# Optimization experiments

Hardware: AMD Instinct MI355X
Metric: run time of the kernel (lower is better)

## Reference

```python
import jax, jax.numpy as jnp
import numpy as np

EMBED = 1024
HEADS = 16
HEAD_DIM = EMBED // HEADS
HIDDEN = int(EMBED * 4.0)
EPS = 1e-6


def setup_inputs() -> dict:
    key = jax.random.key(0)
    ks = jax.random.split(key, 8)
    s = lambda fan_in: 1.0 / np.sqrt(fan_in)
    x = jax.random.normal(ks[0], (2, 2048, EMBED), dtype=jnp.float32)
    return {
        "x": x,
        "ln1_g": jnp.ones((EMBED,), jnp.float32),
        "ln1_b": jnp.zeros((EMBED,), jnp.float32),
        "w_qkv": jax.random.normal(ks[1], (EMBED, 3 * EMBED), jnp.float32) * s(EMBED),
        "b_qkv": jnp.zeros((3 * EMBED,), jnp.float32),
        "w_proj": jax.random.normal(ks[2], (EMBED, EMBED), jnp.float32) * s(EMBED),
        "b_proj": jnp.zeros((EMBED,), jnp.float32),
        "ln2_g": jnp.ones((EMBED,), jnp.float32),
        "ln2_b": jnp.zeros((EMBED,), jnp.float32),
        "w_fc1": jax.random.normal(ks[3], (EMBED, HIDDEN), jnp.float32) * s(EMBED),
        "b_fc1": jnp.zeros((HIDDEN,), jnp.float32),
        "w_fc2": jax.random.normal(ks[4], (HIDDEN, EMBED), jnp.float32) * s(HIDDEN),
        "b_fc2": jnp.zeros((EMBED,), jnp.float32),
    }


def _layernorm(x, g, b):
    mu = jnp.mean(x, axis=-1, keepdims=True)
    var = jnp.mean(jnp.square(x - mu), axis=-1, keepdims=True)
    return (x - mu) * jax.lax.rsqrt(var + EPS) * g + b


def _attention(x, w_qkv, b_qkv, w_proj, b_proj):
    B, N, C = x.shape
    qkv = x @ w_qkv + b_qkv                      # [B,N,3C]
    qkv = qkv.reshape(B, N, 3, HEADS, HEAD_DIM)
    q, k, v = (qkv[:, :, 0], qkv[:, :, 1], qkv[:, :, 2])  # [B,N,H,Dh]
    scale = HEAD_DIM ** -0.5
    attn = jnp.einsum('bnhd,bmhd->bhnm', q, k) * scale     # [B,H,N,N]
    attn = jax.nn.softmax(attn, axis=-1)
    out = jnp.einsum('bhnm,bmhd->bnhd', attn, v).reshape(B, N, C)
    return out @ w_proj + b_proj


def reference(x, ln1_g, ln1_b, w_qkv, b_qkv, w_proj, b_proj,
              ln2_g, ln2_b, w_fc1, b_fc1, w_fc2, b_fc2):
    x = x + _attention(_layernorm(x, ln1_g, ln1_b), w_qkv, b_qkv, w_proj, b_proj)
    h = _layernorm(x, ln2_g, ln2_b)
    h = jax.nn.gelu(h @ w_fc1 + b_fc1, approximate=False)
    x = x + (h @ w_fc2 + b_fc2)
    return x
```

## Files before the change

### kernel.cpp

```cpp
#include <hip/hip_runtime.h>
#include <hip/hip_bf16.h>
#include <math.h>

typedef __bf16 bf16x8 __attribute__((ext_vector_type(8)));
typedef __bf16 bf16x4 __attribute__((ext_vector_type(4)));
typedef unsigned short u16x8 __attribute__((ext_vector_type(8)));
typedef float f32x4 __attribute__((ext_vector_type(4)));

#define EP_QKV 0
#define EP_GELU 1
#define EP_RES 2

static __device__ __forceinline__ unsigned short f2bf(float x) {
  unsigned int u = __float_as_uint(x);
  unsigned int r = (u + 0x7fffu + ((u >> 16) & 1u)) >> 16;
  return (unsigned short)r;
}

static __device__ __forceinline__ unsigned int pkbf(float lo, float hi) {
  return __builtin_amdgcn_perm(__float_as_uint(hi), __float_as_uint(lo), 0x07060302);
}

static __device__ __forceinline__ void async16(const void* g, void* l) {
  __builtin_amdgcn_global_load_lds((__attribute__((address_space(1))) void*)g,
                                   (__attribute__((address_space(3))) void*)l, 16, 0, 0);
}

__global__ __launch_bounds__(256) void wt_transpose(const float* __restrict__ in,
                                                    unsigned short* __restrict__ out,
                                                    int K, int N) {
  __shared__ float tile[32][33];
  const int n0 = blockIdx.x * 32;
  const int k0 = blockIdx.y * 32;
  const int tx = threadIdx.x;
  const int ty = threadIdx.y;
  #pragma unroll
  for (int i = ty; i < 32; i += 8)
    tile[i][tx] = in[(size_t)(k0 + i) * N + n0 + tx];
  __syncthreads();
  #pragma unroll
  for (int i = ty; i < 32; i += 8)
    out[(size_t)(n0 + i) * K + k0 + tx] = f2bf(tile[tx][i]);
}

__global__ __launch_bounds__(256) void ln_kernel(const float* __restrict__ x,
                                                 const float* __restrict__ g,
                                                 const float* __restrict__ b,
                                                 unsigned short* __restrict__ outp) {
  const int row = blockIdx.x;
  const int tid = threadIdx.x;
  const int wave = tid >> 6, lane = tid & 63;
  const float4 v = ((const float4*)(x + (size_t)row * 1024))[tid];
  float s = v.x + v.y + v.z + v.w;
  #pragma unroll
  for (int i = 1; i < 64; i <<= 1) s += __shfl_xor(s, i);
  __shared__ float red[4];
  if (lane == 0) red[wave] = s;
  __syncthreads();
  const float mean = (red[0] + red[1] + red[2] + red[3]) * (1.f / 1024.f);
  const float dx = v.x - mean, dy = v.y - mean, dz = v.z - mean, dw = v.w - mean;
  float ss = dx * dx + dy * dy + dz * dz + dw * dw;
  #pragma unroll
  for (int i = 1; i < 64; i <<= 1) ss += __shfl_xor(ss, i);
  __syncthreads();
  if (lane == 0) red[wave] = ss;
  __syncthreads();
  const float var = (red[0] + red[1] + red[2] + red[3]) * (1.f / 1024.f);
  const float inv = rsqrtf(var + 1e-6f);
  const float4 gv = ((const float4*)g)[tid];
  const float4 bv = ((const float4*)b)[tid];
  ushort4 o;
  o.x = f2bf(dx * inv * gv.x + bv.x);
  o.y = f2bf(dy * inv * gv.y + bv.y);
  o.z = f2bf(dz * inv * gv.z + bv.z);
  o.w = f2bf(dw * inv * gv.w + bv.w);
  ((ushort4*)(outp + (size_t)row * 1024))[tid] = o;
}

template <int TN>
__global__ __launch_bounds__(256) void gemm_kernel(
    const unsigned short* __restrict__ A,
    const unsigned short* __restrict__ BT,
    const float* __restrict__ bias,
    int M, int N, int K, int mode,
    void* __restrict__ outp, const float* __restrict__ res) {
  constexpr int AM = (TN == 128) ? 4 : 2;
  constexpr int BCH = TN / 64;
  __shared__ __align__(16) char smem[16384 + 2 * TN * 64];

  const int tid = threadIdx.x;
  const int wave = tid >> 6, lane = tid & 63;
  const int quad = lane >> 4, l16 = lane & 15;
  const int wm = (TN == 128) ? (wave >> 1) : wave;
  const int wn = (TN == 128) ? (wave & 1) : 0;
  const int bn = blockIdx.x, bm = blockIdx.y;
  const int row_m = bm * 128, row_n = bn * TN;

  int ar[2], ac[2];
  #pragma unroll
  for (int i = 0; i < 2; ++i) {
    const int c = wave * 128 + i * 64 + lane;
    ar[i] = c >> 2;
    ac[i] = ((c & 3) ^ (ar[i] & 3)) * 8;
  }
  int br[BCH], bc[BCH];
  #pragma unroll
  for (int i = 0; i < BCH; ++i) {
    const int c = wave * (64 * BCH) + i * 64 + lane;
    br[i] = c >> 2;
    bc[i] = ((c & 3) ^ (br[i] & 3)) * 8;
  }

  const unsigned short* Ag = A + (size_t)row_m * K;
  const unsigned short* Bg = BT + (size_t)row_n * K;

  const f32x4 z = {0.f, 0.f, 0.f, 0.f};
  f32x4 acc[AM][4];
  #pragma unroll
  for (int i = 0; i < AM; ++i)
    #pragma unroll
    for (int j = 0; j < 4; ++j) acc[i][j] = z;

  auto issue = [&](int kt, int b) {
    unsigned short* As = (unsigned short*)(smem + b * 8192);
    unsigned short* Bs = (unsigned short*)(smem + 16384 + b * TN * 64);
    #pragma unroll
    for (int i = 0; i < 2; ++i)
      async16(Ag + (size_t)ar[i] * K + kt + ac[i], As + wave * 1024 + i * 512);
    #pragma unroll
    for (int i = 0; i < BCH; ++i)
      async16(Bg + (size_t)br[i] * K + kt + bc[i], Bs + wave * (BCH * 512) + i * 512);
  };

  issue(0, 0);
  for (int kt = 0; kt < K; kt += 32) {
    const int b = (kt >> 5) & 1;
    __syncthreads();
    if (kt + 32 < K) issue(kt + 32, b ^ 1);
    const unsigned short* As = (const unsigned short*)(smem + b * 8192);
    const unsigned short* Bs = (const unsigned short*)(smem + 16384 + b * TN * 64);
    bf16x8 af[AM], bfv[4];
    #pragma unroll
    for (int t = 0; t < AM; ++t) {
      const int row = wm * (AM * 16) + t * 16 + l16;
      const int ch = quad ^ (row & 3);
      af[t] = *(const bf16x8*)(As + row * 32 + ch * 8);
    }
    #pragma unroll
    for (int t = 0; t < 4; ++t) {
      const int row = wn * 64 + t * 16 + l16;
      const int ch = quad ^ (row & 3);
      bfv[t] = *(const bf16x8*)(Bs + row * 32 + ch * 8);
    }
    #pragma unroll
    for (int tm = 0; tm < AM; ++tm)
      #pragma unroll
      for (int tn = 0; tn < 4; ++tn)
        acc[tm][tn] = __builtin_amdgcn_mfma_f32_16x16x32_bf16(af[tm], bfv[tn], acc[tm][tn], 0, 0, 0);
  }

  #pragma unroll
  for (int tn = 0; tn < 4; ++tn) {
    const int col = row_n + wn * 64 + tn * 16 + l16;
    const float bv = bias[col];
    #pragma unroll
    for (int tm = 0; tm < AM; ++tm) {
      const int rbase = row_m + wm * (AM * 16) + tm * 16 + quad * 4;
      float v[4];
      #pragma unroll
      for (int r = 0; r < 4; ++r) v[r] = acc[tm][tn][r] + bv;
      if (mode == EP_QKV) {
        unsigned short* outw = (unsigned short*)outp;
        const int which = col >> 10;
        const int h = (col >> 6) & 15, d = col & 63;
        const int bb = rbase >> 11, n = rbase & 2047;
        const size_t bh = (size_t)(bb * 16 + h);
        if (which == 0) {
          #pragma unroll
          for (int r = 0; r < 4; ++r)
            outw[(bh * 2048 + n + r) * 64 + d] = f2bf(v[r] * 0.125f);
        } else if (which == 1) {
          #pragma unroll
          for (int r = 0; r < 4; ++r)
            outw[4194304ull + (bh * 2048 + n + r) * 64 + d] = f2bf(v[r]);
        } else {
          uint2 o;
          o.x = pkbf(v[0], v[1]);
          o.y = pkbf(v[2], v[3]);
          *(uint2*)(outw + 8388608ull + (bh * 64 + d) * 2048 + n) = o;
        }
      } else if (mode == EP_GELU) {
        #pragma unroll
        for (int r = 0; r < 4; ++r) {
          const float u = v[r];
          const float c = 1.5957691216f * fmaf(0.044715f * u * u, u, u);
          const float e = __expf(c);
          const float gl = u - __fdividef(u, e + 1.0f);
          ((unsigned short*)outp)[(size_t)(rbase + r) * N + col] = f2bf(gl);
        }
      } else {
        #pragma unroll
        for (int r = 0; r < 4; ++r)
          ((float*)outp)[(size_t)(rbase + r) * N + col] =
              res[(size_t)(rbase + r) * N + col] + v[r];
      }
    }
  }
}

__global__ __launch_bounds__(256) void attn_kernel(
    const unsigned short* __restrict__ Q,
    const unsigned short* __restrict__ Kb,
    const unsigned short* __restrict__ VT,
    unsigned short* __restrict__ outp) {
  __shared__ __align__(16) char smem[40960];
  unsigned short* Qs = (unsigned short*)smem;
  unsigned short* Ks = (unsigned short*)(smem + 8192);
  unsigned short* Vs = (unsigned short*)(smem + 24576);

  const int tid = threadIdx.x;
  const int wave = tid >> 6, lane = tid & 63;
  const int quad = lane >> 4, l16 = lane & 15;
  const int bhi = blockIdx.y;
  const int q0 = blockIdx.x * 64;

  const unsigned short* Qg = Q + ((size_t)bhi * 2048 + q0) * 64;
  const unsigned short* Kg = Kb + (size_t)bhi * 2048 * 64;
  const unsigned short* Vg = VT + (size_t)bhi * 64 * 2048;

  {
    const int c0 = wave * 128 + lane;
    const int r0 = c0 >> 3, k0 = ((c0 & 7) ^ (r0 & 7)) * 8;
    const int c1 = c0 + 64;
    const int r1 = c1 >> 3, k1 = ((c1 & 7) ^ (r1 & 7)) * 8;
    async16(Qg + r0 * 64 + k0, Qs + wave * 1024);
    async16(Qg + r1 * 64 + k1, Qs + wave * 1024 + 512);
  }
  __syncthreads();

  bf16x8 qb[4][2];
  #pragma unroll
  for (int nt = 0; nt < 4; ++nt)
    #pragma unroll
    for (int h = 0; h < 2; ++h) {
      const int row = nt * 16 + l16;
      const int ch = (h * 4 + quad) ^ (row & 7);
      qb[nt][h] = *(const bf16x8*)(Qs + row * 64 + ch * 8);
    }

  int kr[4], kc[4], vr[4], vc[4];
  #pragma unroll
  for (int i = 0; i < 4; ++i) {
    const int c = wave * 256 + i * 64 + lane;
    kr[i] = c >> 3;
    kc[i] = ((c & 7) ^ (kr[i] & 7)) * 8;
    vr[i] = c >> 4;
    vc[i] = ((c & 15) ^ (vr[i] & 15)) * 8;
  }

  const f32x4 z = {0.f, 0.f, 0.f, 0.f};
  f32x4 acc[4][4];
  #pragma unroll
  for (int i = 0; i < 4; ++i)
    #pragma unroll
    for (int j = 0; j < 4; ++j) acc[i][j] = z;
  float lsum[4] = {0.f, 0.f, 0.f, 0.f};

  const int rowA = wave * 16 + l16;
  const int rowB = 64 + rowA;
  const int swk = l16 & 7;

  for (int kt = 0; kt < 2048; kt += 128) {
    #pragma unroll
    for (int i = 0; i < 4; ++i)
      async16(Kg + (size_t)(kt + kr[i]) * 64 + kc[i], Ks + wave * 2048 + i * 512);
    #pragma unroll
    for (int i = 0; i < 4; ++i)
      async16(Vg + (size_t)vr[i] * 2048 + kt + vc[i], Vs + wave * 2048 + i * 512);
    __syncthreads();

    f32x4 sA[4], sB[4];
    #pragma unroll
    for (int nt = 0; nt < 4; ++nt) { sA[nt] = z; sB[nt] = z; }
    #pragma unroll
    for (int h = 0; h < 2; ++h) {
      const int ch = (h * 4 + quad) ^ swk;
      bf16x8 kfA = *(const bf16x8*)(Ks + rowA * 64 + ch * 8);
      bf16x8 kfB = *(const bf16x8*)(Ks + rowB * 64 + ch * 8);
      #pragma unroll
      for (int nt = 0; nt < 4; ++nt) {
        sA[nt] = __builtin_amdgcn_mfma_f32_16x16x32_bf16(kfA, qb[nt][h], sA[nt], 0, 0, 0);
        sB[nt] = __builtin_amdgcn_mfma_f32_16x16x32_bf16(kfB, qb[nt][h], sB[nt], 0, 0, 0);
      }
    }

    bf16x8 pb[4];
    #pragma unroll
    for (int nt = 0; nt < 4; ++nt) {
      union { unsigned int d[4]; bf16x8 b; } cv;
      float pa[4], pv[4];
      float ls = 0.f;
      #pragma unroll
      for (int r = 0; r < 4; ++r) {
        pa[r] = __expf(sA[nt][r] - 16.0f);
        pv[r] = __expf(sB[nt][r] - 16.0f);
        ls += pa[r] + pv[r];
      }
      cv.d[0] = pkbf(pa[0], pa[1]);
      cv.d[1] = pkbf(pa[2], pa[3]);
      cv.d[2] = pkbf(pv[0], pv[1]);
      cv.d[3] = pkbf(pv[2], pv[3]);
      lsum[nt] += ls;
      pb[nt] = cv.b;
    }

    #pragma unroll
    for (int mt = 0; mt < 4; ++mt) {
      const int d = mt * 16 + l16;
      const int cA = (wave * 2 + (quad >> 1)) ^ (d & 15);
      const int cB = (8 + wave * 2 + (quad >> 1)) ^ (d & 15);
      const int sub = (quad & 1) * 4;
      bf16x4 vA = *(const bf16x4*)(Vs + d * 128 + cA * 8 + sub);
      bf16x4 vB = *(const bf16x4*)(Vs + d * 128 + cB * 8 + sub);
      bf16x8 vf = __builtin_shufflevector(vA, vB, 0, 1, 2, 3, 4, 5, 6, 7);
      #pragma unroll
      for (int nt = 0; nt < 4; ++nt)
        acc[mt][nt] = __builtin_amdgcn_mfma_f32_16x16x32_bf16(vf, pb[nt], acc[mt][nt], 0, 0, 0);
    }
    __syncthreads();
  }

  float* sc = (float*)smem;
  float* lred = (float*)(smem + 32768);
  #pragma unroll
  for (int nt = 0; nt < 4; ++nt) {
    float ls = lsum[nt];
    ls += __shfl_xor(ls, 16);
    ls += __shfl_xor(ls, 32);
    if (quad == 0) lred[wave * 64 + nt * 16 + l16] = ls;
  }
  if (wave >= 2) {
    float* dst = sc + (wave - 2) * 4096;
    #pragma unroll
    for (int mt = 0; mt < 4; ++mt)
      #pragma unroll
      for (int nt = 0; nt < 4; ++nt)
        *(f32x4*)(dst + (mt * 4 + nt) * 256 + lane * 4) = acc[mt][nt];
  }
  __syncthreads();
  if (wave < 2) {
    const float* src = sc + wave * 4096;
    #pragma unroll
    for (int mt = 0; mt < 4; ++mt)
      #pragma unroll
      for (int nt = 0; nt < 4; ++nt)
        acc[mt][nt] += *(const f32x4*)(src + (mt * 4 + nt) * 256 + lane * 4);
  }
  if (wave == 1) {
    float* dst = sc + 4096;
    #pragma unroll
    for (int mt = 0; mt < 4; ++mt)
      #pragma unroll
      for (int nt = 0; nt < 4; ++nt)
        *(f32x4*)(dst + (mt * 4 + nt) * 256 + lane * 4) = acc[mt][nt];
  }
  __syncthreads();
  if (wave == 0) {
    const float* src = sc + 4096;
    float linv[4];
    #pragma unroll
    for (int nt = 0; nt < 4; ++nt) {
      const int qi = nt * 16 + l16;
      const float l = lred[qi] + lred[64 + qi] + lred[128 + qi] + lred[192 + qi];
      linv[nt] = 1.0f / l;
    }
    const int b = bhi >> 4, h = bhi & 15;
    #pragma unroll
    for (int mt = 0; mt < 4; ++mt)
      #pragma unroll
      for (int nt = 0; nt < 4; ++nt) {
        f32x4 o = acc[mt][nt] + *(const f32x4*)(src + (mt * 4 + nt) * 256 + lane * 4);
        uint2 ov;
        ov.x = pkbf(o[0] * linv[nt], o[1] * linv[nt]);
        ov.y = pkbf(o[2] * linv[nt], o[3] * linv[nt]);
        *(uint2*)(outp + ((size_t)(b * 2048 + q0 + nt * 16 + l16)) * 1024 +
                  h * 64 + mt * 16 + quad * 4) = ov;
      }
  }
}

extern "C" void kernel_launch(void* const* d_in, const int* in_sizes, int n_in,
                              void* d_out, int out_size, void* d_ws, size_t ws_size,
                              hipStream_t stream) {
  (void)in_sizes; (void)n_in; (void)out_size; (void)ws_size;
  const float* x      = (const float*)d_in[0];
  const float* ln1_g  = (const float*)d_in[1];
  const float* ln1_b  = (const float*)d_in[2];
  const float* w_qkv  = (const float*)d_in[3];
  const float* b_qkv  = (const float*)d_in[4];
  const float* w_proj = (const float*)d_in[5];
  const float* b_proj = (const float*)d_in[6];
  const float* ln2_g  = (const float*)d_in[7];
  const float* ln2_b  = (const float*)d_in[8];
  const float* w_fc1  = (const float*)d_in[9];
  const float* b_fc1  = (const float*)d_in[10];
  const float* w_fc2  = (const float*)d_in[11];
  const float* b_fc2  = (const float*)d_in[12];

  char* ws = (char*)d_ws;
  unsigned short* wqkvT  = (unsigned short*)(ws + 0);
  unsigned short* wprojT = (unsigned short*)(ws + 6291456);
  unsigned short* wfc1T  = (unsigned short*)(ws + 8388608);
  unsigned short* wfc2T  = (unsigned short*)(ws + 16777216);
  unsigned short* lnb    = (unsigned short*)(ws + 25165824);
  unsigned short* qkvb   = (unsigned short*)(ws + 33554432);
  unsigned short* attnb  = (unsigned short*)(ws + 58720256);
  float*          x2     = (float*)(ws + 67108864);
  unsigned short* hbuf   = qkvb;

  dim3 tb(32, 8);
  wt_transpose<<<dim3(96, 32), tb, 0, stream>>>(w_qkv, wqkvT, 1024, 3072);
  wt_transpose<<<dim3(32, 32), tb, 0, stream>>>(w_proj, wprojT, 1024, 1024);
  wt_transpose<<<dim3(128, 32), tb, 0, stream>>>(w_fc1, wfc1T, 1024, 4096);
  wt_transpose<<<dim3(32, 128), tb, 0, stream>>>(w_fc2, wfc2T, 4096, 1024);

  ln_kernel<<<4096, 256, 0, stream>>>(x, ln1_g, ln1_b, lnb);

  gemm_kernel<128><<<dim3(24, 32), 256, 0, stream>>>(lnb, wqkvT, b_qkv, 4096, 3072, 1024,
                                                     EP_QKV, (void*)qkvb, nullptr);

  attn_kernel<<<dim3(32, 32), 256, 0, stream>>>(qkvb, qkvb + 4194304, qkvb + 8388608, attnb);

  gemm_kernel<64><<<dim3(16, 32), 256, 0, stream>>>(attnb, wprojT, b_proj, 4096, 1024, 1024,
                                                    EP_RES, (void*)x2, x);

  ln_kernel<<<4096, 256, 0, stream>>>(x2, ln2_g, ln2_b, lnb);

  gemm_kernel<128><<<dim3(32, 32), 256, 0, stream>>>(lnb, wfc1T, b_fc1, 4096, 4096, 1024,
                                                     EP_GELU, (void*)hbuf, nullptr);

  gemm_kernel<64><<<dim3(16, 32), 256, 0, stream>>>(hbuf, wfc2T, b_fc2, 4096, 1024, 4096,
                                                    EP_RES, d_out, x2);
}
```

Baseline: 388.0 us.

## Double-buffer K/V tiles in attention and switch softmax to exp2

The attention kernel now keeps two LDS buffers for the K and V tiles. It issues the async global-to-LDS loads for the next key block before computing the current one, so load latency overlaps with the MFMA and softmax work. The log2(e) factor is folded into the Q scaling in the QKV epilogue, and the softmax uses the native exp2 with a matching shifted constant in place of __expf. Shared memory grows from 40 KB to 72 KB per block, which may lower the number of blocks resident per CU.

New measurement: 375.3 us. -3.3%, faster.

```diff
diff --git a/kernel.cpp b/kernel.cpp
--- a/kernel.cpp
+++ b/kernel.cpp
@@ -178,7 +178,7 @@
         if (which == 0) {
           #pragma unroll
           for (int r = 0; r < 4; ++r)
-            outw[(bh * 2048 + n + r) * 64 + d] = f2bf(v[r] * 0.125f);
+            outw[(bh * 2048 + n + r) * 64 + d] = f2bf(v[r] * 0.18033688011112043f);
         } else if (which == 1) {
           #pragma unroll
           for (int r = 0; r < 4; ++r)
@@ -213,10 +213,10 @@
     const unsigned short* __restrict__ Kb,
     const unsigned short* __restrict__ VT,
     unsigned short* __restrict__ outp) {
-  __shared__ __align__(16) char smem[40960];
+  __shared__ __align__(16) char smem[73728];
   unsigned short* Qs = (unsigned short*)smem;
   unsigned short* Ks = (unsigned short*)(smem + 8192);
-  unsigned short* Vs = (unsigned short*)(smem + 24576);
+  unsigned short* Vs = (unsigned short*)(smem + 40960);
 
   const int tid = threadIdx.x;
   const int wave = tid >> 6, lane = tid & 63;
@@ -236,6 +236,30 @@
     async16(Qg + r0 * 64 + k0, Qs + wave * 1024);
     async16(Qg + r1 * 64 + k1, Qs + wave * 1024 + 512);
   }
+
+  const unsigned short* kp[4];
+  const unsigned short* vp[4];
+  #pragma unroll
+  for (int i = 0; i < 4; ++i) {
+    const int c = wave * 256 + i * 64 + lane;
+    const int krr = c >> 3, kcc = ((c & 7) ^ (krr & 7)) * 8;
+    const int vrr = c >> 4, vcc = ((c & 15) ^ (vrr & 15)) * 8;
+    kp[i] = Kg + (size_t)krr * 64 + kcc;
+    vp[i] = Vg + (size_t)vrr * 2048 + vcc;
+  }
+
+  auto issueKV = [&](int b) {
+    unsigned short* Kd = Ks + b * 8192;
+    unsigned short* Vd = Vs + b * 8192;
+    #pragma unroll
+    for (int i = 0; i < 4; ++i) async16(kp[i], Kd + wave * 2048 + i * 512);
+    #pragma unroll
+    for (int i = 0; i < 4; ++i) async16(vp[i], Vd + wave * 2048 + i * 512);
+    #pragma unroll
+    for (int i = 0; i < 4; ++i) { kp[i] += 8192; vp[i] += 128; }
+  };
+
+  issueKV(0);
   __syncthreads();
 
   bf16x8 qb[4][2];
@@ -248,16 +272,6 @@
       qb[nt][h] = *(const bf16x8*)(Qs + row * 64 + ch * 8);
     }
 
-  int kr[4], kc[4], vr[4], vc[4];
-  #pragma unroll
-  for (int i = 0; i < 4; ++i) {
-    const int c = wave * 256 + i * 64 + lane;
-    kr[i] = c >> 3;
-    kc[i] = ((c & 7) ^ (kr[i] & 7)) * 8;
-    vr[i] = c >> 4;
-    vc[i] = ((c & 15) ^ (vr[i] & 15)) * 8;
-  }
-
   const f32x4 z = {0.f, 0.f, 0.f, 0.f};
   f32x4 acc[4][4];
   #pragma unroll
@@ -269,31 +283,25 @@
   const int rowA = wave * 16 + l16;
   const int rowB = 64 + rowA;
   const int swk = l16 & 7;
-
-  for (int kt = 0; kt < 2048; kt += 128) {
-    #pragma unroll
-    for (int i = 0; i < 4; ++i)
-      async16(Kg + (size_t)(kt + kr[i]) * 64 + kc[i], Ks + wave * 2048 + i * 512);
-    #pragma unroll
-    for (int i = 0; i < 4; ++i)
-      async16(Vg + (size_t)vr[i] * 2048 + kt + vc[i], Vs + wave * 2048 + i * 512);
-    __syncthreads();
-
+  const float C2 = 23.083120654223414f;
+
+  auto compute = [&](int b) {
+    const unsigned short* Ksb = Ks + b * 8192;
+    const unsigned short* Vsb = Vs + b * 8192;
     f32x4 sA[4], sB[4];
     #pragma unroll
     for (int nt = 0; nt < 4; ++nt) { sA[nt] = z; sB[nt] = z; }
     #pragma unroll
     for (int h = 0; h < 2; ++h) {
       const int ch = (h * 4 + quad) ^ swk;
-      bf16x8 kfA = *(const bf16x8*)(Ks + rowA * 64 + ch * 8);
-      bf16x8 kfB = *(const bf16x8*)(Ks + rowB * 64 + ch * 8);
+      bf16x8 kfA = *(const bf16x8*)(Ksb + rowA * 64 + ch * 8);
+      bf16x8 kfB = *(const bf16x8*)(Ksb + rowB * 64 + ch * 8);
       #pragma unroll
       for (int nt = 0; nt < 4; ++nt) {
         sA[nt] = __builtin_amdgcn_mfma_f32_16x16x32_bf16(kfA, qb[nt][h], sA[nt], 0, 0, 0);
         sB[nt] = __builtin_amdgcn_mfma_f32_16x16x32_bf16(kfB, qb[nt][h], sB[nt], 0, 0, 0);
       }
     }
-
     bf16x8 pb[4];
     #pragma unroll
     for (int nt = 0; nt < 4; ++nt) {
@@ -302,8 +310,8 @@
       float ls = 0.f;
       #pragma unroll
       for (int r = 0; r < 4; ++r) {
-        pa[r] = __expf(sA[nt][r] - 16.0f);
-        pv[r] = __expf(sB[nt][r] - 16.0f);
+        pa[r] = __builtin_amdgcn_exp2f(sA[nt][r] - C2);
+        pv[r] = __builtin_amdgcn_exp2f(sB[nt][r] - C2);
         ls += pa[r] + pv[r];
       }
       cv.d[0] = pkbf(pa[0], pa[1]);
@@ -313,22 +321,30 @@
       lsum[nt] += ls;
       pb[nt] = cv.b;
     }
-
     #pragma unroll
     for (int mt = 0; mt < 4; ++mt) {
       const int d = mt * 16 + l16;
       const int cA = (wave * 2 + (quad >> 1)) ^ (d & 15);
       const int cB = (8 + wave * 2 + (quad >> 1)) ^ (d & 15);
       const int sub = (quad & 1) * 4;
-      bf16x4 vA = *(const bf16x4*)(Vs + d * 128 + cA * 8 + sub);
-      bf16x4 vB = *(const bf16x4*)(Vs + d * 128 + cB * 8 + sub);
+      bf16x4 vA = *(const bf16x4*)(Vsb + d * 128 + cA * 8 + sub);
+      bf16x4 vB = *(const bf16x4*)(Vsb + d * 128 + cB * 8 + sub);
       bf16x8 vf = __builtin_shufflevector(vA, vB, 0, 1, 2, 3, 4, 5, 6, 7);
       #pragma unroll
       for (int nt = 0; nt < 4; ++nt)
         acc[mt][nt] = __builtin_amdgcn_mfma_f32_16x16x32_bf16(vf, pb[nt], acc[mt][nt], 0, 0, 0);
     }
+  };
+
+  issueKV(1);
+  compute(0);
+  for (int t = 1; t < 16; ++t) {
+    const int b = t & 1;
     __syncthreads();
-  }
+    if (t + 1 < 16) issueKV(b ^ 1);
+    compute(b);
+  }
+  __syncthreads();
 
   float* sc = (float*)smem;
   float* lred = (float*)(smem + 32768);
```
